# Performance work log

Hardware: AMD Instinct MI355X
Metric: run time of the kernel (lower is better)

## Reference

```python
import jax, jax.numpy as jnp
import numpy as np

ANCHORS = np.array([[10,13],[16,30],[33,23],[30,61],[62,45],[59,119],[116,90],[156,198],[373,326]], np.float32)
ANCHOR_MASK = [[6, 7, 8], [3, 4, 5], [0, 1, 2]]
INPUT_SHAPE = np.array([416, 416], np.float32)  # (h, w)
NUM_CLASSES = 80
EPS = 1e-7


def _bce(pred, target):
    # clip_by_tensor + binary cross entropy, as in the torch module
    p = jnp.clip(pred, EPS, 1.0 - EPS)
    return -target * jnp.log(p) - (1.0 - target) * jnp.log(1.0 - p)


def _box_iou(b1, b2):
    # b1: (..., 1, 4), b2: (..., n, 4), center-format xywh (normalized)
    b1_xy, b1_wh = b1[..., :2], b1[..., 2:4]
    b2_xy, b2_wh = b2[..., :2], b2[..., 2:4]
    b1_min, b1_max = b1_xy - b1_wh / 2.0, b1_xy + b1_wh / 2.0
    b2_min, b2_max = b2_xy - b2_wh / 2.0, b2_xy + b2_wh / 2.0
    inter_wh = jnp.maximum(jnp.minimum(b1_max, b2_max) - jnp.maximum(b1_min, b2_min), 0.0)
    inter = inter_wh[..., 0] * inter_wh[..., 1]
    a1 = b1_wh[..., 0] * b1_wh[..., 1]
    a2 = b2_wh[..., 0] * b2_wh[..., 1]
    return inter / (a1 + a2 - inter)


def _decode(y_pred, anchors):
    # y_pred: (b, 3*(5+C), h, w) -> raw: (b, 3, h, w, 5+C)
    b, _, h, w = y_pred.shape
    raw = y_pred.reshape(b, 3, 5 + NUM_CLASSES, h, w).transpose(0, 1, 3, 4, 2)
    gy, gx = jnp.meshgrid(jnp.arange(h, dtype=y_pred.dtype), jnp.arange(w, dtype=y_pred.dtype), indexing='ij')
    grid_xy = jnp.stack([gx, gy], axis=-1)  # (h, w, 2)
    pred_xy = jax.nn.sigmoid(raw[..., 0:2])
    pred_wh = raw[..., 2:4]                 # raw tw, th (MSE'd against log target)
    pred_conf = jax.nn.sigmoid(raw[..., 4:5])
    pred_class = jax.nn.sigmoid(raw[..., 5:])
    # decoded, normalized boxes for IoU-based negative mining
    box_xy = (pred_xy + grid_xy) / jnp.array([w, h], y_pred.dtype)
    box_wh = jnp.exp(pred_wh) * anchors.reshape(3, 1, 1, 2) / jnp.asarray(INPUT_SHAPE[::-1].copy())
    pred_box = jnp.concatenate([box_xy, box_wh], axis=-1)  # (b,3,h,w,4)
    return grid_xy, pred_box, pred_xy, pred_wh, pred_conf, pred_class


def _layer_loss(y_pred, y_true, target, anchors):
    b, _, h, w = y_pred.shape
    grid_xy, pred_box, pred_xy, pred_wh, pred_conf, pred_class = _decode(y_pred, anchors)
    object_mask = y_true[..., 4:5]
    true_xy = y_true[..., 0:2] * jnp.array([h, w], y_pred.dtype) - grid_xy
    true_wh = jnp.log(y_true[..., 2:4] * jnp.asarray(INPUT_SHAPE[::-1].copy()) / anchors.reshape(3, 1, 1, 2))
    true_wh = jnp.where(object_mask > 0, true_wh, jnp.zeros_like(true_wh))
    loss_scale = 2.0 - y_true[..., 2:3] * y_true[..., 3:4]
    # negative mask: every grid/anchor prediction vs all true boxes of its image (vectorized over batch)
    iou = _box_iou(pred_box[:, :, :, :, None, :], target[:, None, None, None, :, :4])  # (b,3,h,w,n)
    best_iou = jnp.max(iou, axis=-1)
    neg = (best_iou < 0.5).astype(y_pred.dtype)[..., None]
    neg_mask = (1.0 - object_mask) * neg
    loss_xy = jnp.sum(object_mask * loss_scale * _bce(pred_xy, true_xy))
    loss_wh = jnp.sum(object_mask * loss_scale * 0.5 * (pred_wh - true_wh) ** 2)
    conf_bce = _bce(pred_conf, object_mask)
    loss_conf = jnp.sum(object_mask * conf_bce) + jnp.sum(neg_mask * conf_bce)
    loss_cls = jnp.sum(object_mask * _bce(pred_class, y_true[..., 5:]))
    return loss_xy + loss_wh + loss_conf + loss_cls


def setup_inputs() -> dict:
    key = jax.random.key(0)
    ks = jax.random.split(key, 7)
    grids = [13, 26, 52]
    b, n = 32, 20
    inp = {}
    for i, g in enumerate(grids):
        inp[f'y_pred{i}'] = jax.random.normal(ks[i], (b, 3 * (5 + NUM_CLASSES), g, g), jnp.float32)
        # y_true values in (0.05, 0.95): keeps log(true_wh) and 1/y_true grads bounded
        inp[f'y_true{i}'] = 0.05 + 0.9 * jax.random.uniform(ks[3 + i], (b, 3, g, g, 5 + NUM_CLASSES), jnp.float32)
    inp['target'] = 0.05 + 0.9 * jax.random.uniform(ks[6], (b, n, 5), jnp.float32)
    return inp


def reference(y_pred0, y_pred1, y_pred2, y_true0, y_true1, y_true2, target):
    total = jnp.zeros((), jnp.float32)
    for yp, yt, mask in ((y_pred0, y_true0, ANCHOR_MASK[0]),
                         (y_pred1, y_true1, ANCHOR_MASK[1]),
                         (y_pred2, y_true2, ANCHOR_MASK[2])):
        total = total + _layer_loss(yp, yt, target, jnp.asarray(ANCHORS[mask]))
    return total
```

## Files before the change

### kernel.cpp

```cpp
#include <hip/hip_runtime.h>
#include <math.h>

#define BLOCK 256
#define NB0 64
#define NB1 254
#define NB2 1014
#define NBLOCKS (NB0 + NB1 + NB2)

__constant__ float c_anch[9][2] = {
    {116.f, 90.f}, {156.f, 198.f}, {373.f, 326.f},
    { 30.f, 61.f}, { 62.f,  45.f}, { 59.f, 119.f},
    { 10.f, 13.f}, { 16.f,  30.f}, { 33.f,  23.f}
};

__device__ __forceinline__ float softplusf(float x) {
    float ax = fabsf(x);
    return fmaxf(x, 0.f) + __logf(1.f + __expf(-ax));
}

__device__ __forceinline__ float sigmoidf(float x) {
    return __fdividef(1.f, 1.f + __expf(-x));
}

__global__ __launch_bounds__(BLOCK) void yolo_loss_main(
    const float* __restrict__ p0, const float* __restrict__ p1, const float* __restrict__ p2,
    const float* __restrict__ t0, const float* __restrict__ t1, const float* __restrict__ t2,
    const float* __restrict__ tgt, float* __restrict__ partials)
{
    int blk = blockIdx.x;
    const float* pred;
    const float* tru;
    int layer, g, cells, bbase;
    if (blk < NB0)            { layer = 0; pred = p0; tru = t0; g = 13; cells = 16224;  bbase = 0; }
    else if (blk < NB0 + NB1) { layer = 1; pred = p1; tru = t1; g = 26; cells = 64896;  bbase = NB0; }
    else                      { layer = 2; pred = p2; tru = t2; g = 52; cells = 259584; bbase = NB0 + NB1; }

    int idx = (blk - bbase) * BLOCK + threadIdx.x;
    float acc = 0.f;

    if (idx < cells) {
        int hw = g * g;
        int ij = idx % hw;
        int a  = (idx / hw) % 3;
        int b  = idx / (3 * hw);
        int i  = ij / g;
        int j  = ij - i * g;

        const float* pb = pred + (size_t)((b * 3 + a) * 85) * hw + ij;
        const float* tb = tru + (size_t)((b * 3 + a) * hw + ij) * 85;

        float r0 = pb[0];
        float r1 = pb[hw];
        float r2 = pb[2 * hw];
        float r3 = pb[3 * hw];
        float r4 = pb[4 * hw];

        float y0 = tb[0], y1 = tb[1], y2 = tb[2], y3 = tb[3], mask = tb[4];

        float gf = (float)g, gx = (float)j, gy = (float)i;
        float aw = c_anch[layer * 3 + a][0];
        float ah = c_anch[layer * 3 + a][1];

        float true_x = y0 * gf - gx;
        float true_y = y1 * gf - gy;
        float ls = 2.f - y2 * y3;
        float lxy = (softplusf(r0) - true_x * r0) + (softplusf(r1) - true_y * r1);
        acc += mask * ls * lxy;

        float tw = __logf(y2 * (416.f / aw));
        float th = __logf(y3 * (416.f / ah));
        float dw = r2 - tw, dh = r3 - th;
        acc += mask * ls * 0.5f * (dw * dw + dh * dh);

        float cbce = softplusf(r4) - mask * r4;

        float sx = sigmoidf(r0);
        float sy = sigmoidf(r1);
        float bx = __fdividef(sx + gx, gf);
        float by = __fdividef(sy + gy, gf);
        float bw = __expf(r2) * aw * (1.f / 416.f);
        float bh = __expf(r3) * ah * (1.f / 416.f);
        float a1 = bw * bh;
        float b1minx = bx - 0.5f * bw, b1maxx = bx + 0.5f * bw;
        float b1miny = by - 0.5f * bh, b1maxy = by + 0.5f * bh;

        const float* tg = tgt + b * 20 * 5;
        float best = 0.f;
#pragma unroll 4
        for (int k = 0; k < 20; k++) {
            float tx  = tg[k * 5 + 0];
            float ty  = tg[k * 5 + 1];
            float tww = tg[k * 5 + 2];
            float thh = tg[k * 5 + 3];
            float iw = fminf(b1maxx, tx + 0.5f * tww) - fmaxf(b1minx, tx - 0.5f * tww);
            float ih = fminf(b1maxy, ty + 0.5f * thh) - fmaxf(b1miny, ty - 0.5f * thh);
            iw = fmaxf(iw, 0.f);
            ih = fmaxf(ih, 0.f);
            float inter = iw * ih;
            float iou = __fdividef(inter, a1 + tww * thh - inter);
            best = fmaxf(best, iou);
        }
        float neg = (best < 0.5f) ? 1.f : 0.f;
        acc += mask * cbce + (1.f - mask) * neg * cbce;

        float cls = 0.f;
#pragma unroll 8
        for (int c = 0; c < 80; c++) {
            float x = pb[(5 + c) * hw];
            float t = tb[5 + c];
            cls += softplusf(x) - t * x;
        }
        acc += mask * cls;
    }

    for (int off = 32; off > 0; off >>= 1)
        acc += __shfl_down(acc, off, 64);
    __shared__ float sh[BLOCK / 64];
    if ((threadIdx.x & 63) == 0)
        sh[threadIdx.x >> 6] = acc;
    __syncthreads();
    if (threadIdx.x == 0) {
        float s = 0.f;
        for (int wv = 0; wv < BLOCK / 64; wv++) s += sh[wv];
        partials[blockIdx.x] = s;
    }
}

__global__ __launch_bounds__(BLOCK) void yolo_loss_reduce(
    const float* __restrict__ partials, float* __restrict__ out)
{
    float s = 0.f;
    for (int i = threadIdx.x; i < NBLOCKS; i += BLOCK)
        s += partials[i];
    for (int off = 32; off > 0; off >>= 1)
        s += __shfl_down(s, off, 64);
    __shared__ float sh[BLOCK / 64];
    if ((threadIdx.x & 63) == 0)
        sh[threadIdx.x >> 6] = s;
    __syncthreads();
    if (threadIdx.x == 0) {
        float tot = 0.f;
        for (int wv = 0; wv < BLOCK / 64; wv++) tot += sh[wv];
        out[0] = tot;
    }
}

extern "C" void kernel_launch(void* const* d_in, const int* in_sizes, int n_in,
                              void* d_out, int out_size, void* d_ws, size_t ws_size,
                              hipStream_t stream) {
    const float* p0  = (const float*)d_in[0];
    const float* t0  = (const float*)d_in[1];
    const float* p1  = (const float*)d_in[2];
    const float* t1  = (const float*)d_in[3];
    const float* p2  = (const float*)d_in[4];
    const float* t2  = (const float*)d_in[5];
    const float* tgt = (const float*)d_in[6];
    float* partials  = (float*)d_ws;

    yolo_loss_main<<<NBLOCKS, BLOCK, 0, stream>>>(p0, p1, p2, t0, t1, t2, tgt, partials);
    yolo_loss_reduce<<<1, BLOCK, 0, stream>>>(partials, (float*)d_out);
}
```

Before: 261.4 us.

## Vectorize y_true loads and replace reduce kernel with atomic accumulation

The 80-class loop now reads y_true in float4 chunks and uses four independent accumulators. This cuts load instruction count on the strided per-cell AoS layout and breaks the serial add chain. The separate reduce kernel is removed. Each block instead atomically adds its partial sum into the output, which is zeroed with an async memset. Risks: the float4 loads at tb and tb+5 are only 4-byte aligned for most cells, and atomic summation makes the floating-point result order nondeterministic.

```diff
diff --git a/kernel.cpp b/kernel.cpp
--- a/kernel.cpp
+++ b/kernel.cpp
@@ -6,6 +6,8 @@
 #define NB1 254
 #define NB2 1014
 #define NBLOCKS (NB0 + NB1 + NB2)
+
+typedef float f4 __attribute__((ext_vector_type(4)));
 
 __constant__ float c_anch[9][2] = {
     {116.f, 90.f}, {156.f, 198.f}, {373.f, 326.f},
@@ -25,7 +27,7 @@
 __global__ __launch_bounds__(BLOCK) void yolo_loss_main(
     const float* __restrict__ p0, const float* __restrict__ p1, const float* __restrict__ p2,
     const float* __restrict__ t0, const float* __restrict__ t1, const float* __restrict__ t2,
-    const float* __restrict__ tgt, float* __restrict__ partials)
+    const float* __restrict__ tgt, float* __restrict__ out)
 {
     int blk = blockIdx.x;
     const float* pred;
@@ -55,7 +57,9 @@
         float r3 = pb[3 * hw];
         float r4 = pb[4 * hw];
 
-        float y0 = tb[0], y1 = tb[1], y2 = tb[2], y3 = tb[3], mask = tb[4];
+        f4 y = *reinterpret_cast<const f4*>(tb);
+        float y0 = y.x, y1 = y.y, y2 = y.z, y3 = y.w;
+        float mask = tb[4];
 
         float gf = (float)g, gx = (float)j, gy = (float)i;
         float aw = c_anch[layer * 3 + a][0];
@@ -103,14 +107,22 @@
         float neg = (best < 0.5f) ? 1.f : 0.f;
         acc += mask * cbce + (1.f - mask) * neg * cbce;
 
-        float cls = 0.f;
-#pragma unroll 8
-        for (int c = 0; c < 80; c++) {
-            float x = pb[(5 + c) * hw];
-            float t = tb[5 + c];
-            cls += softplusf(x) - t * x;
+        const f4* t4 = reinterpret_cast<const f4*>(tb + 5);
+        float c0 = 0.f, c1 = 0.f, c2 = 0.f, c3 = 0.f;
+#pragma unroll 5
+        for (int k = 0; k < 20; k++) {
+            f4 t = t4[k];
+            const float* px = pb + (5 + 4 * k) * hw;
+            float x0 = px[0];
+            float x1 = px[hw];
+            float x2 = px[2 * hw];
+            float x3 = px[3 * hw];
+            c0 += softplusf(x0) - t.x * x0;
+            c1 += softplusf(x1) - t.y * x1;
+            c2 += softplusf(x2) - t.z * x2;
+            c3 += softplusf(x3) - t.w * x3;
         }
-        acc += mask * cls;
+        acc += mask * ((c0 + c1) + (c2 + c3));
     }
 
     for (int off = 32; off > 0; off >>= 1)
@@ -122,26 +134,7 @@
     if (threadIdx.x == 0) {
         float s = 0.f;
         for (int wv = 0; wv < BLOCK / 64; wv++) s += sh[wv];
-        partials[blockIdx.x] = s;
-    }
-}
-
-__global__ __launch_bounds__(BLOCK) void yolo_loss_reduce(
-    const float* __restrict__ partials, float* __restrict__ out)
-{
-    float s = 0.f;
-    for (int i = threadIdx.x; i < NBLOCKS; i += BLOCK)
-        s += partials[i];
-    for (int off = 32; off > 0; off >>= 1)
-        s += __shfl_down(s, off, 64);
-    __shared__ float sh[BLOCK / 64];
-    if ((threadIdx.x & 63) == 0)
-        sh[threadIdx.x >> 6] = s;
-    __syncthreads();
-    if (threadIdx.x == 0) {
-        float tot = 0.f;
-        for (int wv = 0; wv < BLOCK / 64; wv++) tot += sh[wv];
-        out[0] = tot;
+        atomicAdd(out, s);
     }
 }
 
@@ -155,8 +148,7 @@
     const float* p2  = (const float*)d_in[4];
     const float* t2  = (const float*)d_in[5];
     const float* tgt = (const float*)d_in[6];
-    float* partials  = (float*)d_ws;
 
-    yolo_loss_main<<<NBLOCKS, BLOCK, 0, stream>>>(p0, p1, p2, t0, t1, t2, tgt, partials);
-    yolo_loss_reduce<<<1, BLOCK, 0, stream>>>(partials, (float*)d_out);
+    hipMemsetAsync(d_out, 0, sizeof(float), stream);
+    yolo_loss_main<<<NBLOCKS, BLOCK, 0, stream>>>(p0, p1, p2, t0, t1, t2, tgt, (float*)d_out);
 }
```

Measured after the change: 294.4 us. 12.6% more time.
